# Kernel tuning notes

Measured on AMD Instinct MI355X. Metric: run time of the kernel, lower is better.

The kernel has to match this reference:

```python
import jax, jax.numpy as jnp
import numpy as np

N = 100000       # nodes
E = 1600000      # edges (before self-loops)
IN = 32          # input_dim
HID = 64         # hidden_dim
HEADS = 4
HO = HID // HEADS  # per-head out of gat1
OUT = 32         # output_dim
HID2 = HID // 2
BN_EPS = 1e-5
NEG_SLOPE = 0.2  # PyG GATConv default leaky relu slope


def setup_inputs() -> dict:
    key = jax.random.key(0)
    ks = jax.random.split(key, 28)
    f32 = jnp.float32
    rn = lambda k, s, sc=0.1: jax.random.normal(k, s, f32) * sc
    inp = {}
    inp["x"] = jax.random.normal(ks[0], (N, IN), f32)
    inp["edge_index"] = jax.random.randint(ks[1], (2, E), 0, N, jnp.int32)
    # GATConv 1: in=IN, heads=HEADS, out/head=HO, concat
    inp["W1"] = rn(ks[2], (IN, HEADS * HO))
    inp["att_src1"] = rn(ks[3], (HEADS, HO))
    inp["att_dst1"] = rn(ks[4], (HEADS, HO))
    inp["b1"] = rn(ks[5], (HEADS * HO,))
    # GATConv 2: in=HID, heads=1, out=OUT, no concat (mean)
    inp["W2"] = rn(ks[6], (HID, OUT))
    inp["att_src2"] = rn(ks[7], (1, OUT))
    inp["att_dst2"] = rn(ks[8], (1, OUT))
    inp["b2"] = rn(ks[9], (OUT,))
    # BatchNorms (inference mode: running stats)
    inp["bn1_g"] = jnp.ones((HID,), f32)
    inp["bn1_b"] = jnp.zeros((HID,), f32)
    inp["bn1_m"] = rn(ks[10], (HID,), 0.1)
    inp["bn1_v"] = jax.random.uniform(ks[11], (HID,), f32, 0.5, 1.5)
    inp["bn2_g"] = jnp.ones((OUT,), f32)
    inp["bn2_b"] = jnp.zeros((OUT,), f32)
    inp["bn2_m"] = rn(ks[12], (OUT,), 0.1)
    inp["bn2_v"] = jax.random.uniform(ks[13], (OUT,), f32, 0.5, 1.5)
    # classifier: OUT -> HID2 -> 3
    inp["cls_w1"] = rn(ks[14], (OUT, HID2))
    inp["cls_b1"] = rn(ks[15], (HID2,))
    inp["cls_w2"] = rn(ks[16], (HID2, 3))
    inp["cls_b2"] = rn(ks[17], (3,))
    inp["reg_w1"] = rn(ks[18], (OUT, HID2))
    inp["reg_b1"] = rn(ks[19], (HID2,))
    inp["reg_w2"] = rn(ks[20], (HID2, 1))
    inp["reg_b2"] = rn(ks[21], (1,))
    return inp


def _segment_softmax(e, seg, n):
    # e: [E, H]; softmax over edges sharing the same destination segment
    m = jax.ops.segment_max(e, seg, num_segments=n)
    ex = jnp.exp(e - m[seg])
    s = jax.ops.segment_sum(ex, seg, num_segments=n)
    return ex / (s[seg] + 1e-16)


def _gat(x, src, dst, W, a_src, a_dst, b, heads, ho, concat):
    n = x.shape[0]
    h = (x @ W).reshape(n, heads, ho)                    # [N,H,F]
    e = (h * a_src).sum(-1)[src] + (h * a_dst).sum(-1)[dst]  # [E,H]
    e = jax.nn.leaky_relu(e, NEG_SLOPE)
    alpha = _segment_softmax(e, dst, n)                  # [E,H]
    out = jax.ops.segment_sum(h[src] * alpha[:, :, None], dst, num_segments=n)
    out = out.reshape(n, heads * ho) if concat else out.mean(axis=1)
    return out + b


def _bn(x, g, b, m, v):
    return (x - m) * jax.lax.rsqrt(v + BN_EPS) * g + b


def reference(x, edge_index, W1, att_src1, att_dst1, b1, W2, att_src2, att_dst2, b2,
              bn1_g, bn1_b, bn1_m, bn1_v, bn2_g, bn2_b, bn2_m, bn2_v,
              cls_w1, cls_b1, cls_w2, cls_b2, reg_w1, reg_b1, reg_w2, reg_b2):
    n = x.shape[0]
    # PyG GATConv default add_self_loops=True
    loops = jnp.arange(n, dtype=edge_index.dtype)
    src = jnp.concatenate([edge_index[0], loops])
    dst = jnp.concatenate([edge_index[1], loops])

    h = _gat(x, src, dst, W1, att_src1, att_dst1, b1, HEADS, HO, True)   # [N, HID]
    h = jax.nn.relu(_bn(h, bn1_g, bn1_b, bn1_m, bn1_v))
    emb = _gat(h, src, dst, W2, att_src2, att_dst2, b2, 1, OUT, False)   # [N, OUT]
    emb = jax.nn.relu(_bn(emb, bn2_g, bn2_b, bn2_m, bn2_v))

    roles = jax.nn.relu(emb @ cls_w1 + cls_b1) @ cls_w2 + cls_b2          # [N, 3]
    energy = jax.nn.relu(emb @ reg_w1 + reg_b1) @ reg_w2 + reg_b2         # [N, 1]
    return emb, roles, energy
```

## Files before the change

kernel.cpp:

```cpp
#include <hip/hip_runtime.h>
#include <hip/hip_bf16.h>

#define NN 100000
#define EE 1600000
#define ETOT (EE + NN)
#define IND 32
#define HIDD 64
#define NHEADS 4
#define OUTD 32
#define HID2D 32
#define LOG2E 1.44269504f

#define BSH 8
#define NBUCK 391
#define CAP 5120
#define EPB 8192

typedef unsigned int uint;

__device__ __forceinline__ uint pack2(float a, float b) {
  uint lo = (uint)__bfloat16_as_ushort(__float2bfloat16(a));
  uint hi = (uint)__bfloat16_as_ushort(__float2bfloat16(b));
  return (hi << 16) | lo;
}
__device__ __forceinline__ float lo2f(uint w) { return __uint_as_float(w << 16); }
__device__ __forceinline__ float hi2r(uint w) { return __uint_as_float(w); }

__global__ __launch_bounds__(256) void k_lin1(
    const float* __restrict__ x, const float* __restrict__ W1,
    const float* __restrict__ atsrc, const float* __restrict__ atdst,
    uint* __restrict__ h1u, float* __restrict__ as1, float* __restrict__ ad1,
    int* __restrict__ bcur) {
  __shared__ float Ws[IND * HIDD];
  __shared__ float xs[8 * IND];
  __shared__ float atS[HIDD], atD[HIDD];
  int t = threadIdx.x;
  if (blockIdx.x == 0) { bcur[t] = 0; bcur[t + 256] = 0; }
  for (int i = t; i < IND * HIDD; i += 256) Ws[i] = W1[i];
  if (t < HIDD) { atS[t] = atsrc[t]; atD[t] = atdst[t]; }
  xs[t] = x[blockIdx.x * 256 + t];
  __syncthreads();
  int nl = t >> 5, tl = t & 31;
  int node = blockIdx.x * 8 + nl;
  int j0 = 2 * tl, j1 = j0 + 1;
  float a0 = 0.f, a1 = 0.f;
#pragma unroll
  for (int k = 0; k < IND; k++) {
    float xv = xs[nl * IND + k];
    a0 += xv * Ws[k * HIDD + j0];
    a1 += xv * Ws[k * HIDD + j1];
  }
  h1u[node * 32 + tl] = pack2(a0, a1);
  float ps = a0 * atS[j0] + a1 * atS[j1];
  float pd = a0 * atD[j0] + a1 * atD[j1];
#pragma unroll
  for (int off = 4; off >= 1; off >>= 1) {
    ps += __shfl_down(ps, off, 8);
    pd += __shfl_down(pd, off, 8);
  }
  if ((tl & 7) == 0) {
    as1[node * NHEADS + (tl >> 3)] = ps * LOG2E;
    ad1[node * NHEADS + (tl >> 3)] = pd * LOG2E;
  }
}

__global__ __launch_bounds__(256) void k_lin2(
    const float* __restrict__ hbn, const float* __restrict__ W2,
    const float* __restrict__ atsrc, const float* __restrict__ atdst,
    uint* __restrict__ h2u, float* __restrict__ as2, float* __restrict__ ad2) {
  __shared__ float Ws[HIDD * OUTD];
  __shared__ float xs[16 * HIDD];
  __shared__ float atS[OUTD], atD[OUTD];
  int t = threadIdx.x;
  for (int i = t; i < HIDD * OUTD; i += 256) Ws[i] = W2[i];
  if (t < OUTD) { atS[t] = atsrc[t]; atD[t] = atdst[t]; }
  for (int i = t; i < 16 * HIDD; i += 256) xs[i] = hbn[blockIdx.x * 16 * HIDD + i];
  __syncthreads();
  int nl = t >> 4, tl = t & 15;
  int node = blockIdx.x * 16 + nl;
  int j0 = 2 * tl, j1 = j0 + 1;
  float a0 = 0.f, a1 = 0.f;
#pragma unroll
  for (int k = 0; k < HIDD; k++) {
    float xv = xs[nl * HIDD + k];
    a0 += xv * Ws[k * OUTD + j0];
    a1 += xv * Ws[k * OUTD + j1];
  }
  h2u[node * 16 + tl] = pack2(a0, a1);
  float ps = a0 * atS[j0] + a1 * atS[j1];
  float pd = a0 * atD[j0] + a1 * atD[j1];
#pragma unroll
  for (int off = 8; off >= 1; off >>= 1) {
    ps += __shfl_down(ps, off, 16);
    pd += __shfl_down(pd, off, 16);
  }
  if (tl == 0) { as2[node] = ps * LOG2E; ad2[node] = pd * LOG2E; }
}

__global__ __launch_bounds__(256) void k_bin(const int* __restrict__ ei,
                                             int* __restrict__ bcur,
                                             int* __restrict__ bins) {
  __shared__ int cnt[NBUCK];
  int t = threadIdx.x;
  for (int i = t; i < NBUCK; i += 256) cnt[i] = 0;
  __syncthreads();
  int base = blockIdx.x * EPB;
  int lim = base + EPB; if (lim > ETOT) lim = ETOT;
  for (int i = base + t; i < lim; i += 256) {
    int d = (i < EE) ? ei[EE + i] : (i - EE);
    atomicAdd(&cnt[d >> BSH], 1);
  }
  __syncthreads();
  for (int i = t; i < NBUCK; i += 256) cnt[i] = atomicAdd(&bcur[i], cnt[i]);
  __syncthreads();
  for (int i = base + t; i < lim; i += 256) {
    int s, d;
    if (i < EE) { s = ei[i]; d = ei[EE + i]; } else { s = i - EE; d = s; }
    int bk = d >> BSH;
    int pos = atomicAdd(&cnt[bk], 1);
    bins[bk * CAP + pos] = (s << BSH) | (d & ((1 << BSH) - 1));
  }
}

__global__ __launch_bounds__(256) void k_csr(const int* __restrict__ bcur,
                                             const int* __restrict__ bins,
                                             int* __restrict__ rowp,
                                             int* __restrict__ srcs) {
  __shared__ int lrec[CAP];
  __shared__ int sA[512], sB[512];
  __shared__ int ldeg[256];
  int b = blockIdx.x, t = threadIdx.x;
  if (b == 0 && t == 0) rowp[NN] = ETOT;
  sA[t] = (t < NBUCK) ? bcur[t] : 0;
  sA[t + 256] = (t + 256 < NBUCK) ? bcur[t + 256] : 0;
  __syncthreads();
  int* in = sA; int* out = sB;
  for (int off = 1; off < 512; off <<= 1) {
    for (int i = t; i < 512; i += 256)
      out[i] = in[i] + ((i >= off) ? in[i - off] : 0);
    __syncthreads();
    int* tmp = in; in = out; out = tmp;
  }
  int gb = (b == 0) ? 0 : in[b - 1];
  __syncthreads();
  int count = bcur[b]; if (count > CAP) count = CAP;
  ldeg[t] = 0;
  __syncthreads();
  for (int i = t; i < count; i += 256) {
    int r = bins[b * CAP + i];
    lrec[i] = r;
    atomicAdd(&ldeg[r & 255], 1);
  }
  __syncthreads();
  int dv = ldeg[t];
  sA[t] = dv;
  __syncthreads();
  in = sA; out = sB;
  for (int off = 1; off < 256; off <<= 1) {
    out[t] = in[t] + ((t >= off) ? in[t - off] : 0);
    __syncthreads();
    int* tmp = in; in = out; out = tmp;
  }
  int nb = b << BSH;
  int ex = in[t] - dv;
  if (nb + t < NN) rowp[nb + t] = gb + ex;
  ldeg[t] = ex;
  __syncthreads();
  for (int i = t; i < count; i += 256) {
    int r = lrec[i];
    int pos = atomicAdd(&ldeg[r & 255], 1);
    srcs[gb + pos] = (r >> BSH) << 3;
  }
}

__global__ __launch_bounds__(256, 4) void k_agg1(
    const int* __restrict__ rowp, const int* __restrict__ srcs,
    const uint* __restrict__ h1u, const float* __restrict__ as1,
    const float* __restrict__ ad1, const float* __restrict__ b1,
    const float* __restrict__ g, const float* __restrict__ bb,
    const float* __restrict__ m, const float* __restrict__ v,
    float* __restrict__ hbn) {
  int t = threadIdx.x;
  int wid = t >> 6, lane = t & 63;
  int n0 = blockIdx.x * 16 + wid * 4;
  int slot = lane >> 3;
  int fl = lane & 7;
  int hd = fl >> 1;
  int rp[5];
#pragma unroll
  for (int k = 0; k < 5; k++) rp[k] = rowp[n0 + k];
  const uint4* h14 = (const uint4*)h1u;
  float acc[4][8], l[4], adv[4], as[4];
  int p[4], p1[4], lp[4], en[4], s1v[4];
  uint4 w[4];
#pragma unroll
  for (int k = 0; k < 4; k++) {
    adv[k] = ad1[(n0 + k) * NHEADS + hd];
    en[k] = rp[k + 1];
    lp[k] = en[k] - 1;
    p[k] = rp[k] + slot;
    int pc = p[k] < lp[k] ? p[k] : lp[k];
    int s0 = srcs[pc];
    w[k] = h14[s0 + fl];
    as[k] = as1[(s0 >> 1) + hd];
    p1[k] = p[k] + 8;
    int pc1 = p1[k] < lp[k] ? p1[k] : lp[k];
    s1v[k] = srcs[pc1];
    l[k] = 0.f;
#pragma unroll
    for (int i = 0; i < 8; i++) acc[k][i] = 0.f;
  }
  while (p[0] < en[0] || p[1] < en[1] || p[2] < en[2] || p[3] < en[3]) {
    uint4 wn[4]; float an[4]; int s2[4];
#pragma unroll
    for (int k = 0; k < 4; k++) {
      wn[k] = h14[s1v[k] + fl];
      an[k] = as1[(s1v[k] >> 1) + hd];
      int p2 = p1[k] + 8;
      int pc = p2 < lp[k] ? p2 : lp[k];
      s2[k] = srcs[pc];
    }
#pragma unroll
    for (int k = 0; k < 4; k++) {
      if (p[k] < en[k]) {
        float e = as[k] + adv[k];
        e = fmaxf(e, 0.2f * e);
        float ex = exp2f(e);
        l[k] += ex;
        acc[k][0] += ex * lo2f(w[k].x); acc[k][1] += ex * hi2r(w[k].x);
        acc[k][2] += ex * lo2f(w[k].y); acc[k][3] += ex * hi2r(w[k].y);
        acc[k][4] += ex * lo2f(w[k].z); acc[k][5] += ex * hi2r(w[k].z);
        acc[k][6] += ex * lo2f(w[k].w); acc[k][7] += ex * hi2r(w[k].w);
      }
      w[k] = wn[k]; as[k] = an[k]; s1v[k] = s2[k];
      p[k] = p1[k]; p1[k] += 8;
    }
  }
#pragma unroll
  for (int off = 8; off <= 32; off <<= 1) {
#pragma unroll
    for (int k = 0; k < 4; k++) {
#pragma unroll
      for (int i = 0; i < 8; i++) acc[k][i] += __shfl_xor(acc[k][i], off, 64);
      l[k] += __shfl_xor(l[k], off, 64);
    }
  }
  if (slot < 4) {
    float lsum = 0.f, av[8];
#pragma unroll
    for (int i = 0; i < 8; i++) av[i] = 0.f;
#pragma unroll
    for (int k = 0; k < 4; k++) {
      if (slot == k) {
        lsum = l[k];
#pragma unroll
        for (int i = 0; i < 8; i++) av[i] = acc[k][i];
      }
    }
    int node = n0 + slot;
    float li = 1.f / (lsum + 1e-16f);
    int fb = fl * 8;
    float o[8];
#pragma unroll
    for (int i = 0; i < 8; i++) {
      int j = fb + i;
      float ov = av[i] * li + b1[j];
      ov = (ov - m[j]) * rsqrtf(v[j] + 1e-5f) * g[j] + bb[j];
      o[i] = fmaxf(ov, 0.f);
    }
    float4* dst = (float4*)(hbn + node * HIDD + fb);
    dst[0] = make_float4(o[0], o[1], o[2], o[3]);
    dst[1] = make_float4(o[4], o[5], o[6], o[7]);
  }
}

__global__ __launch_bounds__(256, 4) void k_agg2(
    const int* __restrict__ rowp, const int* __restrict__ srcs,
    const uint* __restrict__ h2u, const float* __restrict__ as2,
    const float* __restrict__ ad2, const float* __restrict__ b2v,
    const float* __restrict__ g, const float* __restrict__ bb,
    const float* __restrict__ m, const float* __restrict__ v,
    float* __restrict__ out_emb) {
  int t = threadIdx.x;
  int wid = t >> 6, lane = t & 63;
  int n0 = blockIdx.x * 16 + wid * 4;
  int slot = lane >> 3;
  int fl = lane & 7;
  int rp[5];
#pragma unroll
  for (int k = 0; k < 5; k++) rp[k] = rowp[n0 + k];
  const uint2* h22 = (const uint2*)h2u;
  float acc[4][4], l[4], adv[4], as[4];
  int p[4], p1[4], lp[4], en[4], s1v[4];
  uint2 w[4];
#pragma unroll
  for (int k = 0; k < 4; k++) {
    adv[k] = ad2[n0 + k];
    en[k] = rp[k + 1];
    lp[k] = en[k] - 1;
    p[k] = rp[k] + slot;
    int pc = p[k] < lp[k] ? p[k] : lp[k];
    int s0 = srcs[pc];
    w[k] = h22[s0 + fl];
    as[k] = as2[s0 >> 3];
    p1[k] = p[k] + 8;
    int pc1 = p1[k] < lp[k] ? p1[k] : lp[k];
    s1v[k] = srcs[pc1];
    l[k] = 0.f;
#pragma unroll
    for (int i = 0; i < 4; i++) acc[k][i] = 0.f;
  }
  while (p[0] < en[0] || p[1] < en[1] || p[2] < en[2] || p[3] < en[3]) {
    uint2 wn[4]; float an[4]; int s2[4];
#pragma unroll
    for (int k = 0; k < 4; k++) {
      wn[k] = h22[s1v[k] + fl];
      an[k] = as2[s1v[k] >> 3];
      int p2 = p1[k] + 8;
      int pc = p2 < lp[k] ? p2 : lp[k];
      s2[k] = srcs[pc];
    }
#pragma unroll
    for (int k = 0; k < 4; k++) {
      if (p[k] < en[k]) {
        float e = as[k] + adv[k];
        e = fmaxf(e, 0.2f * e);
        float ex = exp2f(e);
        l[k] += ex;
        acc[k][0] += ex * lo2f(w[k].x); acc[k][1] += ex * hi2r(w[k].x);
        acc[k][2] += ex * lo2f(w[k].y); acc[k][3] += ex * hi2r(w[k].y);
      }
      w[k] = wn[k]; as[k] = an[k]; s1v[k] = s2[k];
      p[k] = p1[k]; p1[k] += 8;
    }
  }
#pragma unroll
  for (int off = 8; off <= 32; off <<= 1) {
#pragma unroll
    for (int k = 0; k < 4; k++) {
#pragma unroll
      for (int i = 0; i < 4; i++) acc[k][i] += __shfl_xor(acc[k][i], off, 64);
      l[k] += __shfl_xor(l[k], off, 64);
    }
  }
  if (slot < 4) {
    float lsum = 0.f, av[4];
#pragma unroll
    for (int i = 0; i < 4; i++) av[i] = 0.f;
#pragma unroll
    for (int k = 0; k < 4; k++) {
      if (slot == k) {
        lsum = l[k];
#pragma unroll
        for (int i = 0; i < 4; i++) av[i] = acc[k][i];
      }
    }
    int node = n0 + slot;
    float li = 1.f / (lsum + 1e-16f);
    int fb = fl * 4;
    float o[4];
#pragma unroll
    for (int i = 0; i < 4; i++) {
      int j = fb + i;
      float ov = av[i] * li + b2v[j];
      ov = (ov - m[j]) * rsqrtf(v[j] + 1e-5f) * g[j] + bb[j];
      o[i] = fmaxf(ov, 0.f);
    }
    *(float4*)(out_emb + node * OUTD + fb) = make_float4(o[0], o[1], o[2], o[3]);
  }
}

__global__ __launch_bounds__(256) void k_mlp(
    const float* __restrict__ embf,
    const float* __restrict__ cw1, const float* __restrict__ cb1,
    const float* __restrict__ cw2, const float* __restrict__ cb2,
    const float* __restrict__ rw1, const float* __restrict__ rb1,
    const float* __restrict__ rw2, const float* __restrict__ rb2,
    float* __restrict__ out_roles, float* __restrict__ out_energy) {
  __shared__ float C1[OUTD * HID2D], R1[OUTD * HID2D];
  __shared__ float C2[HID2D * 3], CB1[HID2D], RB1[HID2D], R2[HID2D];
  __shared__ float CB2v[3], RB2v;
  int t = threadIdx.x;
  for (int i = t; i < OUTD * HID2D; i += 256) { C1[i] = cw1[i]; R1[i] = rw1[i]; }
  if (t < HID2D) { CB1[t] = cb1[t]; RB1[t] = rb1[t]; R2[t] = rw2[t]; }
  if (t < HID2D * 3) C2[t] = cw2[t];
  if (t < 3) CB2v[t] = cb2[t];
  if (t == 0) RB2v = rb2[0];
  __syncthreads();
  int node = blockIdx.x * 256 + t;
  if (node >= NN) return;
  float e[OUTD];
#pragma unroll
  for (int k = 0; k < OUTD; k++) e[k] = embf[node * OUTD + k];
  float r0 = CB2v[0], r1 = CB2v[1], r2 = CB2v[2], en = RB2v;
  for (int j = 0; j < HID2D; j++) {
    float hc = CB1[j], hr = RB1[j];
#pragma unroll
    for (int k = 0; k < OUTD; k++) {
      hc += e[k] * C1[k * HID2D + j];
      hr += e[k] * R1[k * HID2D + j];
    }
    hc = fmaxf(hc, 0.f);
    hr = fmaxf(hr, 0.f);
    r0 += hc * C2[j * 3 + 0];
    r1 += hc * C2[j * 3 + 1];
    r2 += hc * C2[j * 3 + 2];
    en += hr * R2[j];
  }
  out_roles[node * 3 + 0] = r0;
  out_roles[node * 3 + 1] = r1;
  out_roles[node * 3 + 2] = r2;
  out_energy[node] = en;
}

extern "C" void kernel_launch(void* const* d_in, const int* in_sizes, int n_in,
                              void* d_out, int out_size, void* d_ws, size_t ws_size,
                              hipStream_t stream) {
  const float* x    = (const float*)d_in[0];
  const int*   ei   = (const int*)d_in[1];
  const float* W1   = (const float*)d_in[2];
  const float* as1w = (const float*)d_in[3];
  const float* ad1w = (const float*)d_in[4];
  const float* b1   = (const float*)d_in[5];
  const float* W2   = (const float*)d_in[6];
  const float* as2w = (const float*)d_in[7];
  const float* ad2w = (const float*)d_in[8];
  const float* b2v  = (const float*)d_in[9];
  const float* bn1g = (const float*)d_in[10];
  const float* bn1b = (const float*)d_in[11];
  const float* bn1m = (const float*)d_in[12];
  const float* bn1v = (const float*)d_in[13];
  const float* bn2g = (const float*)d_in[14];
  const float* bn2b = (const float*)d_in[15];
  const float* bn2m = (const float*)d_in[16];
  const float* bn2v = (const float*)d_in[17];
  const float* cw1  = (const float*)d_in[18];
  const float* cb1  = (const float*)d_in[19];
  const float* cw2  = (const float*)d_in[20];
  const float* cb2  = (const float*)d_in[21];
  const float* rw1  = (const float*)d_in[22];
  const float* rb1  = (const float*)d_in[23];
  const float* rw2  = (const float*)d_in[24];
  const float* rb2  = (const float*)d_in[25];

  uint*  h1u = (uint*)d_ws;
  float* hbn = (float*)(h1u + NN * 32);
  float* as1 = hbn + NN * HIDD;
  float* ad1 = as1 + NN * NHEADS;
  int* rowp  = (int*)(ad1 + NN * NHEADS);
  int* srcs  = rowp + NN + 1;
  int* bcur  = srcs + ETOT;
  int* bins  = bcur + 512;
  uint* h2u  = h1u;
  float* as2 = as1;
  float* ad2 = ad1;

  float* out        = (float*)d_out;
  float* out_emb    = out;
  float* out_roles  = out + NN * OUTD;
  float* out_energy = out + NN * (OUTD + 3);

  k_lin1<<<NN / 8, 256, 0, stream>>>(x, W1, as1w, ad1w, h1u, as1, ad1, bcur);
  k_bin<<<(ETOT + EPB - 1) / EPB, 256, 0, stream>>>(ei, bcur, bins);
  k_csr<<<NBUCK, 256, 0, stream>>>(bcur, bins, rowp, srcs);
  k_agg1<<<NN / 16, 256, 0, stream>>>(rowp, srcs, h1u, as1, ad1, b1, bn1g, bn1b, bn1m, bn1v, hbn);
  k_lin2<<<NN / 16, 256, 0, stream>>>(hbn, W2, as2w, ad2w, h2u, as2, ad2);
  k_agg2<<<NN / 16, 256, 0, stream>>>(rowp, srcs, h2u, as2, ad2, b2v, bn2g, bn2b, bn2m, bn2v, out_emb);
  k_mlp<<<(NN + 255) / 256, 256, 0, stream>>>(out_emb, cw1, cb1, cw2, cb2, rw1, rb1, rw2, rb2, out_roles, out_energy);
}
```

Baseline: 316.9 us.

## Build CSR with global degree atomics, two-pass scan, and atomic scatter

Result: slower. 475.9 us (+50.2%).

```diff
diff --git a/kernel.cpp b/kernel.cpp
--- a/kernel.cpp
+++ b/kernel.cpp
@@ -11,10 +11,9 @@
 #define HID2D 32
 #define LOG2E 1.44269504f
 
-#define BSH 8
-#define NBUCK 391
-#define CAP 5120
-#define EPB 8192
+#define NBK 391
+#define NNP (NBK * 256)
+#define EGRID ((ETOT + 1023) / 1024)
 
 typedef unsigned int uint;
 
@@ -30,12 +29,13 @@
     const float* __restrict__ x, const float* __restrict__ W1,
     const float* __restrict__ atsrc, const float* __restrict__ atdst,
     uint* __restrict__ h1u, float* __restrict__ as1, float* __restrict__ ad1,
-    int* __restrict__ bcur) {
+    int* __restrict__ deg) {
   __shared__ float Ws[IND * HIDD];
   __shared__ float xs[8 * IND];
   __shared__ float atS[HIDD], atD[HIDD];
   int t = threadIdx.x;
-  if (blockIdx.x == 0) { bcur[t] = 0; bcur[t + 256] = 0; }
+  if (t < 8) deg[(blockIdx.x << 3) + t] = 0;
+  if (blockIdx.x == 0 && t < (NNP - NN)) deg[NN + t] = 0;
   for (int i = t; i < IND * HIDD; i += 256) Ws[i] = W1[i];
   if (t < HIDD) { atS[t] = atsrc[t]; atD[t] = atdst[t]; }
   xs[t] = x[blockIdx.x * 256 + t];
@@ -97,42 +97,45 @@
   if (tl == 0) { as2[node] = ps * LOG2E; ad2[node] = pd * LOG2E; }
 }
 
-__global__ __launch_bounds__(256) void k_bin(const int* __restrict__ ei,
-                                             int* __restrict__ bcur,
-                                             int* __restrict__ bins) {
-  __shared__ int cnt[NBUCK];
-  int t = threadIdx.x;
-  for (int i = t; i < NBUCK; i += 256) cnt[i] = 0;
+__global__ __launch_bounds__(256) void k_deg(const int* __restrict__ ei,
+                                             int* __restrict__ deg) {
+  int i = blockIdx.x * 1024 + threadIdx.x;
+#pragma unroll
+  for (int u = 0; u < 4; u++, i += 256) {
+    if (i < ETOT) {
+      int d = (i < EE) ? ei[EE + i] : (i - EE);
+      atomicAdd(&deg[d], 1);
+    }
+  }
+}
+
+__global__ __launch_bounds__(256) void k_scan1(const int* __restrict__ deg,
+                                               int* __restrict__ lrow,
+                                               int* __restrict__ bsum) {
+  __shared__ int sA[256], sB[256];
+  int b = blockIdx.x, t = threadIdx.x;
+  int n = b * 256 + t;
+  int d = deg[n];
+  sA[t] = d;
   __syncthreads();
-  int base = blockIdx.x * EPB;
-  int lim = base + EPB; if (lim > ETOT) lim = ETOT;
-  for (int i = base + t; i < lim; i += 256) {
-    int d = (i < EE) ? ei[EE + i] : (i - EE);
-    atomicAdd(&cnt[d >> BSH], 1);
-  }
-  __syncthreads();
-  for (int i = t; i < NBUCK; i += 256) cnt[i] = atomicAdd(&bcur[i], cnt[i]);
-  __syncthreads();
-  for (int i = base + t; i < lim; i += 256) {
-    int s, d;
-    if (i < EE) { s = ei[i]; d = ei[EE + i]; } else { s = i - EE; d = s; }
-    int bk = d >> BSH;
-    int pos = atomicAdd(&cnt[bk], 1);
-    bins[bk * CAP + pos] = (s << BSH) | (d & ((1 << BSH) - 1));
-  }
-}
-
-__global__ __launch_bounds__(256) void k_csr(const int* __restrict__ bcur,
-                                             const int* __restrict__ bins,
-                                             int* __restrict__ rowp,
-                                             int* __restrict__ srcs) {
-  __shared__ int lrec[CAP];
+  int* in = sA; int* out = sB;
+  for (int off = 1; off < 256; off <<= 1) {
+    out[t] = in[t] + ((t >= off) ? in[t - off] : 0);
+    __syncthreads();
+    int* tmp = in; in = out; out = tmp;
+  }
+  lrow[n] = in[t] - d;
+  if (t == 255) bsum[b] = in[255];
+}
+
+__global__ __launch_bounds__(256) void k_scan2(const int* __restrict__ bsum,
+                                               const int* __restrict__ lrow,
+                                               int* __restrict__ rowp,
+                                               int* __restrict__ cur) {
   __shared__ int sA[512], sB[512];
-  __shared__ int ldeg[256];
   int b = blockIdx.x, t = threadIdx.x;
-  if (b == 0 && t == 0) rowp[NN] = ETOT;
-  sA[t] = (t < NBUCK) ? bcur[t] : 0;
-  sA[t + 256] = (t + 256 < NBUCK) ? bcur[t + 256] : 0;
+  sA[t] = (t < NBK) ? bsum[t] : 0;
+  sA[t + 256] = (t + 256 < NBK) ? bsum[t + 256] : 0;
   __syncthreads();
   int* in = sA; int* out = sB;
   for (int off = 1; off < 512; off <<= 1) {
@@ -142,34 +145,24 @@
     int* tmp = in; in = out; out = tmp;
   }
   int gb = (b == 0) ? 0 : in[b - 1];
-  __syncthreads();
-  int count = bcur[b]; if (count > CAP) count = CAP;
-  ldeg[t] = 0;
-  __syncthreads();
-  for (int i = t; i < count; i += 256) {
-    int r = bins[b * CAP + i];
-    lrec[i] = r;
-    atomicAdd(&ldeg[r & 255], 1);
-  }
-  __syncthreads();
-  int dv = ldeg[t];
-  sA[t] = dv;
-  __syncthreads();
-  in = sA; out = sB;
-  for (int off = 1; off < 256; off <<= 1) {
-    out[t] = in[t] + ((t >= off) ? in[t - off] : 0);
-    __syncthreads();
-    int* tmp = in; in = out; out = tmp;
-  }
-  int nb = b << BSH;
-  int ex = in[t] - dv;
-  if (nb + t < NN) rowp[nb + t] = gb + ex;
-  ldeg[t] = ex;
-  __syncthreads();
-  for (int i = t; i < count; i += 256) {
-    int r = lrec[i];
-    int pos = atomicAdd(&ldeg[r & 255], 1);
-    srcs[gb + pos] = (r >> BSH) << 3;
+  int n = b * 256 + t;
+  int v = gb + lrow[n];
+  if (n < NN) { rowp[n] = v; cur[n] = v; }
+  else if (n == NN) rowp[NN] = ETOT;
+}
+
+__global__ __launch_bounds__(256) void k_scat(const int* __restrict__ ei,
+                                              int* __restrict__ cur,
+                                              int* __restrict__ srcs) {
+  int i = blockIdx.x * 1024 + threadIdx.x;
+#pragma unroll
+  for (int u = 0; u < 4; u++, i += 256) {
+    if (i < ETOT) {
+      int s, d;
+      if (i < EE) { s = ei[i]; d = ei[EE + i]; } else { s = d = i - EE; }
+      int pos = atomicAdd(&cur[d], 1);
+      srcs[pos] = s << 3;
+    }
   }
 }
 
@@ -449,8 +442,10 @@
   float* ad1 = as1 + NN * NHEADS;
   int* rowp  = (int*)(ad1 + NN * NHEADS);
   int* srcs  = rowp + NN + 1;
-  int* bcur  = srcs + ETOT;
-  int* bins  = bcur + 512;
+  int* deg   = srcs + ETOT;
+  int* lrow  = deg + NNP;
+  int* cur   = lrow + NNP;
+  int* bsum  = cur + NNP;
   uint* h2u  = h1u;
   float* as2 = as1;
   float* ad2 = ad1;
@@ -460,9 +455,11 @@
   float* out_roles  = out + NN * OUTD;
   float* out_energy = out + NN * (OUTD + 3);
 
-  k_lin1<<<NN / 8, 256, 0, stream>>>(x, W1, as1w, ad1w, h1u, as1, ad1, bcur);
-  k_bin<<<(ETOT + EPB - 1) / EPB, 256, 0, stream>>>(ei, bcur, bins);
-  k_csr<<<NBUCK, 256, 0, stream>>>(bcur, bins, rowp, srcs);
+  k_lin1<<<NN / 8, 256, 0, stream>>>(x, W1, as1w, ad1w, h1u, as1, ad1, deg);
+  k_deg<<<EGRID, 256, 0, stream>>>(ei, deg);
+  k_scan1<<<NBK, 256, 0, stream>>>(deg, lrow, bsum);
+  k_scan2<<<NBK, 256, 0, stream>>>(bsum, lrow, rowp, cur);
+  k_scat<<<EGRID, 256, 0, stream>>>(ei, cur, srcs);
   k_agg1<<<NN / 16, 256, 0, stream>>>(rowp, srcs, h1u, as1, ad1, b1, bn1g, bn1b, bn1m, bn1v, hbn);
   k_lin2<<<NN / 16, 256, 0, stream>>>(hbn, W2, as2w, ad2w, h2u, as2, ad2);
   k_agg2<<<NN / 16, 256, 0, stream>>>(rowp, srcs, h2u, as2, ad2, b2v, bn2g, bn2b, bn2m, bn2v, out_emb);
```

## Fuse layer-2 linear projection into first aggregation epilogue

Applied to the files above, without the earlier changes.

After: 324.1 us. +2.3%, slower.

```diff
diff --git a/kernel.cpp b/kernel.cpp
--- a/kernel.cpp
+++ b/kernel.cpp
@@ -64,39 +64,6 @@
   }
 }
 
-__global__ __launch_bounds__(256) void k_lin2(
-    const float* __restrict__ hbn, const float* __restrict__ W2,
-    const float* __restrict__ atsrc, const float* __restrict__ atdst,
-    uint* __restrict__ h2u, float* __restrict__ as2, float* __restrict__ ad2) {
-  __shared__ float Ws[HIDD * OUTD];
-  __shared__ float xs[16 * HIDD];
-  __shared__ float atS[OUTD], atD[OUTD];
-  int t = threadIdx.x;
-  for (int i = t; i < HIDD * OUTD; i += 256) Ws[i] = W2[i];
-  if (t < OUTD) { atS[t] = atsrc[t]; atD[t] = atdst[t]; }
-  for (int i = t; i < 16 * HIDD; i += 256) xs[i] = hbn[blockIdx.x * 16 * HIDD + i];
-  __syncthreads();
-  int nl = t >> 4, tl = t & 15;
-  int node = blockIdx.x * 16 + nl;
-  int j0 = 2 * tl, j1 = j0 + 1;
-  float a0 = 0.f, a1 = 0.f;
-#pragma unroll
-  for (int k = 0; k < HIDD; k++) {
-    float xv = xs[nl * HIDD + k];
-    a0 += xv * Ws[k * OUTD + j0];
-    a1 += xv * Ws[k * OUTD + j1];
-  }
-  h2u[node * 16 + tl] = pack2(a0, a1);
-  float ps = a0 * atS[j0] + a1 * atS[j1];
-  float pd = a0 * atD[j0] + a1 * atD[j1];
-#pragma unroll
-  for (int off = 8; off >= 1; off >>= 1) {
-    ps += __shfl_down(ps, off, 16);
-    pd += __shfl_down(pd, off, 16);
-  }
-  if (tl == 0) { as2[node] = ps * LOG2E; ad2[node] = pd * LOG2E; }
-}
-
 __global__ __launch_bounds__(256) void k_bin(const int* __restrict__ ei,
                                              int* __restrict__ bcur,
                                              int* __restrict__ bins) {
@@ -179,8 +146,18 @@
     const float* __restrict__ ad1, const float* __restrict__ b1,
     const float* __restrict__ g, const float* __restrict__ bb,
     const float* __restrict__ m, const float* __restrict__ v,
-    float* __restrict__ hbn) {
+    const float* __restrict__ W2, const float* __restrict__ atsrc2,
+    const float* __restrict__ atdst2,
+    uint* __restrict__ h2u, float* __restrict__ as2, float* __restrict__ ad2) {
+  __shared__ float W2t[OUTD * HIDD];
+  __shared__ float atS2[OUTD], atD2[OUTD];
   int t = threadIdx.x;
+  for (int i = t; i < OUTD * HIDD; i += 256) {
+    int j = i >> 6, k = i & 63;
+    W2t[i] = W2[k * OUTD + j];
+  }
+  if (t < OUTD) { atS2[t] = atsrc2[t]; atD2[t] = atdst2[t]; }
+  __syncthreads();
   int wid = t >> 6, lane = t & 63;
   int n0 = blockIdx.x * 16 + wid * 4;
   int slot = lane >> 3;
@@ -245,32 +222,63 @@
       l[k] += __shfl_xor(l[k], off, 64);
     }
   }
-  if (slot < 4) {
-    float lsum = 0.f, av[8];
-#pragma unroll
-    for (int i = 0; i < 8; i++) av[i] = 0.f;
-#pragma unroll
-    for (int k = 0; k < 4; k++) {
-      if (slot == k) {
-        lsum = l[k];
-#pragma unroll
-        for (int i = 0; i < 8; i++) av[i] = acc[k][i];
-      }
-    }
-    int node = n0 + slot;
-    float li = 1.f / (lsum + 1e-16f);
-    int fb = fl * 8;
-    float o[8];
+  int s = slot & 3, half = slot >> 2;
+  int node = n0 + s;
+  float lsum = 0.f, av[8];
+#pragma unroll
+  for (int i = 0; i < 8; i++) av[i] = 0.f;
+#pragma unroll
+  for (int k = 0; k < 4; k++) {
+    if (s == k) {
+      lsum = l[k];
+#pragma unroll
+      for (int i = 0; i < 8; i++) av[i] = acc[k][i];
+    }
+  }
+  float li = 1.f / (lsum + 1e-16f);
+  int fb = fl * 8;
+  float o[8];
+#pragma unroll
+  for (int i = 0; i < 8; i++) {
+    int j = fb + i;
+    float ov = av[i] * li + b1[j];
+    ov = (ov - m[j]) * rsqrtf(v[j] + 1e-5f) * g[j] + bb[j];
+    o[i] = fmaxf(ov, 0.f);
+  }
+  float psel0 = 0.f, psel1 = 0.f, ps = 0.f, pd = 0.f;
+#pragma unroll
+  for (int r = 0; r < 8; r++) {
+    int jp = (half << 3) | r;
+    int j0 = jp * 2;
+    float a0 = 0.f, a1 = 0.f;
 #pragma unroll
     for (int i = 0; i < 8; i++) {
-      int j = fb + i;
-      float ov = av[i] * li + b1[j];
-      ov = (ov - m[j]) * rsqrtf(v[j] + 1e-5f) * g[j] + bb[j];
-      o[i] = fmaxf(ov, 0.f);
-    }
-    float4* dst = (float4*)(hbn + node * HIDD + fb);
-    dst[0] = make_float4(o[0], o[1], o[2], o[3]);
-    dst[1] = make_float4(o[4], o[5], o[6], o[7]);
+      a0 += o[i] * W2t[j0 * HIDD + fb + i];
+      a1 += o[i] * W2t[(j0 + 1) * HIDD + fb + i];
+    }
+#pragma unroll
+    for (int off = 1; off <= 4; off <<= 1) {
+      a0 += __shfl_xor(a0, off, 64);
+      a1 += __shfl_xor(a1, off, 64);
+    }
+    if (fl == r) {
+      psel0 = a0; psel1 = a1;
+      ps = a0 * atS2[j0] + a1 * atS2[j0 + 1];
+      pd = a0 * atD2[j0] + a1 * atD2[j0 + 1];
+    }
+  }
+  int jp = (half << 3) | fl;
+  h2u[node * 16 + jp] = pack2(psel0, psel1);
+#pragma unroll
+  for (int off = 1; off <= 4; off <<= 1) {
+    ps += __shfl_xor(ps, off, 64);
+    pd += __shfl_xor(pd, off, 64);
+  }
+  ps += __shfl_xor(ps, 32, 64);
+  pd += __shfl_xor(pd, 32, 64);
+  if (fl == 0 && half == 0) {
+    as2[node] = ps * LOG2E;
+    ad2[node] = pd * LOG2E;
   }
 }
 
@@ -444,16 +452,15 @@
   const float* rb2  = (const float*)d_in[25];
 
   uint*  h1u = (uint*)d_ws;
-  float* hbn = (float*)(h1u + NN * 32);
-  float* as1 = hbn + NN * HIDD;
+  uint*  h2u = h1u + NN * 32;
+  float* as1 = (float*)(h2u + NN * 16);
   float* ad1 = as1 + NN * NHEADS;
-  int* rowp  = (int*)(ad1 + NN * NHEADS);
+  float* as2 = ad1 + NN * NHEADS;
+  float* ad2 = as2 + NN;
+  int* rowp  = (int*)(ad2 + NN);
   int* srcs  = rowp + NN + 1;
   int* bcur  = srcs + ETOT;
   int* bins  = bcur + 512;
-  uint* h2u  = h1u;
-  float* as2 = as1;
-  float* ad2 = ad1;
 
   float* out        = (float*)d_out;
   float* out_emb    = out;
@@ -463,8 +470,8 @@
   k_lin1<<<NN / 8, 256, 0, stream>>>(x, W1, as1w, ad1w, h1u, as1, ad1, bcur);
   k_bin<<<(ETOT + EPB - 1) / EPB, 256, 0, stream>>>(ei, bcur, bins);
   k_csr<<<NBUCK, 256, 0, stream>>>(bcur, bins, rowp, srcs);
-  k_agg1<<<NN / 16, 256, 0, stream>>>(rowp, srcs, h1u, as1, ad1, b1, bn1g, bn1b, bn1m, bn1v, hbn);
-  k_lin2<<<NN / 16, 256, 0, stream>>>(hbn, W2, as2w, ad2w, h2u, as2, ad2);
+  k_agg1<<<NN / 16, 256, 0, stream>>>(rowp, srcs, h1u, as1, ad1, b1, bn1g, bn1b, bn1m, bn1v,
+                                      W2, as2w, ad2w, h2u, as2, ad2);
   k_agg2<<<NN / 16, 256, 0, stream>>>(rowp, srcs, h2u, as2, ad2, b2v, bn2g, bn2b, bn2m, bn2v, out_emb);
   k_mlp<<<(NN + 255) / 256, 256, 0, stream>>>(out_emb, cw1, cb1, cw2, cb2, rw1, rb1, rw2, rb2, out_roles, out_energy);
 }
```

## Register-tile the second GAT linear layer with a transposed, swizzled shared-memory input tile

Applied to the files above, without the earlier changes.

New measurement: 383.2 us. 1.21x slower.

```diff
diff --git a/kernel.cpp b/kernel.cpp
--- a/kernel.cpp
+++ b/kernel.cpp
@@ -15,6 +15,7 @@
 #define NBUCK 391
 #define CAP 5120
 #define EPB 8192
+#define L2NB 128
 
 typedef unsigned int uint;
 
@@ -62,39 +63,6 @@
     as1[node * NHEADS + (tl >> 3)] = ps * LOG2E;
     ad1[node * NHEADS + (tl >> 3)] = pd * LOG2E;
   }
-}
-
-__global__ __launch_bounds__(256) void k_lin2(
-    const float* __restrict__ hbn, const float* __restrict__ W2,
-    const float* __restrict__ atsrc, const float* __restrict__ atdst,
-    uint* __restrict__ h2u, float* __restrict__ as2, float* __restrict__ ad2) {
-  __shared__ float Ws[HIDD * OUTD];
-  __shared__ float xs[16 * HIDD];
-  __shared__ float atS[OUTD], atD[OUTD];
-  int t = threadIdx.x;
-  for (int i = t; i < HIDD * OUTD; i += 256) Ws[i] = W2[i];
-  if (t < OUTD) { atS[t] = atsrc[t]; atD[t] = atdst[t]; }
-  for (int i = t; i < 16 * HIDD; i += 256) xs[i] = hbn[blockIdx.x * 16 * HIDD + i];
-  __syncthreads();
-  int nl = t >> 4, tl = t & 15;
-  int node = blockIdx.x * 16 + nl;
-  int j0 = 2 * tl, j1 = j0 + 1;
-  float a0 = 0.f, a1 = 0.f;
-#pragma unroll
-  for (int k = 0; k < HIDD; k++) {
-    float xv = xs[nl * HIDD + k];
-    a0 += xv * Ws[k * OUTD + j0];
-    a1 += xv * Ws[k * OUTD + j1];
-  }
-  h2u[node * 16 + tl] = pack2(a0, a1);
-  float ps = a0 * atS[j0] + a1 * atS[j1];
-  float pd = a0 * atD[j0] + a1 * atD[j1];
-#pragma unroll
-  for (int off = 8; off >= 1; off >>= 1) {
-    ps += __shfl_down(ps, off, 16);
-    pd += __shfl_down(pd, off, 16);
-  }
-  if (tl == 0) { as2[node] = ps * LOG2E; ad2[node] = pd * LOG2E; }
 }
 
 __global__ __launch_bounds__(256) void k_bin(const int* __restrict__ ei,
@@ -271,6 +239,76 @@
     float4* dst = (float4*)(hbn + node * HIDD + fb);
     dst[0] = make_float4(o[0], o[1], o[2], o[3]);
     dst[1] = make_float4(o[4], o[5], o[6], o[7]);
+  }
+}
+
+__global__ __launch_bounds__(256) void k_lin2(
+    const float* __restrict__ hbn, const float* __restrict__ W2,
+    const float* __restrict__ atsrc, const float* __restrict__ atdst,
+    uint* __restrict__ h2u, float* __restrict__ as2, float* __restrict__ ad2) {
+  __shared__ float xsT[HIDD][L2NB];
+  __shared__ float Wp[HIDD * OUTD];
+  __shared__ float atS[OUTD], atD[OUTD];
+  int t = threadIdx.x;
+  int nb = blockIdx.x * L2NB;
+  for (int i = t; i < HIDD * OUTD; i += 256) Wp[i] = W2[i];
+  if (t < OUTD) { atS[t] = atsrc[t]; atD[t] = atdst[t]; }
+#pragma unroll
+  for (int i = 0; i < 8; i++) {
+    int idx = t + i * 256;
+    int node = idx >> 4, c = idx & 15;
+    int gnode = nb + node;
+    float4 vv = make_float4(0.f, 0.f, 0.f, 0.f);
+    if (gnode < NN) vv = ((const float4*)hbn)[gnode * 16 + c];
+    int ns = node ^ ((c & 7) << 2);
+    xsT[4 * c + 0][ns] = vv.x;
+    xsT[4 * c + 1][ns] = vv.y;
+    xsT[4 * c + 2][ns] = vv.z;
+    xsT[4 * c + 3][ns] = vv.w;
+  }
+  __syncthreads();
+  int w = t >> 6, lane = t & 63;
+  int gq = lane >> 3, tl = lane & 7;
+  int base = w * 32 + gq * 4;
+  int j0 = tl * 4;
+  float acc[4][4];
+#pragma unroll
+  for (int e = 0; e < 4; e++)
+#pragma unroll
+    for (int d = 0; d < 4; d++) acc[e][d] = 0.f;
+#pragma unroll
+  for (int k = 0; k < HIDD; k++) {
+    float4 wv = *(const float4*)&Wp[k * OUTD + j0];
+    int swz = ((k >> 2) & 7) << 2;
+    float4 xv = *(const float4*)&xsT[k][base ^ swz];
+    acc[0][0] += xv.x * wv.x; acc[0][1] += xv.x * wv.y;
+    acc[0][2] += xv.x * wv.z; acc[0][3] += xv.x * wv.w;
+    acc[1][0] += xv.y * wv.x; acc[1][1] += xv.y * wv.y;
+    acc[1][2] += xv.y * wv.z; acc[1][3] += xv.y * wv.w;
+    acc[2][0] += xv.z * wv.x; acc[2][1] += xv.z * wv.y;
+    acc[2][2] += xv.z * wv.z; acc[2][3] += xv.z * wv.w;
+    acc[3][0] += xv.w * wv.x; acc[3][1] += xv.w * wv.y;
+    acc[3][2] += xv.w * wv.z; acc[3][3] += xv.w * wv.w;
+  }
+#pragma unroll
+  for (int e = 0; e < 4; e++) {
+    int node = nb + base + e;
+    float ps = acc[e][0] * atS[j0] + acc[e][1] * atS[j0 + 1] +
+               acc[e][2] * atS[j0 + 2] + acc[e][3] * atS[j0 + 3];
+    float pd = acc[e][0] * atD[j0] + acc[e][1] * atD[j0 + 1] +
+               acc[e][2] * atD[j0 + 2] + acc[e][3] * atD[j0 + 3];
+#pragma unroll
+    for (int off = 1; off <= 4; off <<= 1) {
+      ps += __shfl_xor(ps, off, 64);
+      pd += __shfl_xor(pd, off, 64);
+    }
+    if (node < NN) {
+      uint2 pk;
+      pk.x = pack2(acc[e][0], acc[e][1]);
+      pk.y = pack2(acc[e][2], acc[e][3]);
+      ((uint2*)h2u)[node * 8 + tl] = pk;
+      if (tl == 0) { as2[node] = ps * LOG2E; ad2[node] = pd * LOG2E; }
+    }
   }
 }
 
@@ -464,7 +502,7 @@
   k_bin<<<(ETOT + EPB - 1) / EPB, 256, 0, stream>>>(ei, bcur, bins);
   k_csr<<<NBUCK, 256, 0, stream>>>(bcur, bins, rowp, srcs);
   k_agg1<<<NN / 16, 256, 0, stream>>>(rowp, srcs, h1u, as1, ad1, b1, bn1g, bn1b, bn1m, bn1v, hbn);
-  k_lin2<<<NN / 16, 256, 0, stream>>>(hbn, W2, as2w, ad2w, h2u, as2, ad2);
+  k_lin2<<<(NN + L2NB - 1) / L2NB, 256, 0, stream>>>(hbn, W2, as2w, ad2w, h2u, as2, ad2);
   k_agg2<<<NN / 16, 256, 0, stream>>>(rowp, srcs, h2u, as2, ad2, b2v, bn2g, bn2b, bn2m, bn2v, out_emb);
   k_mlp<<<(NN + 255) / 256, 256, 0, stream>>>(out_emb, cw1, cb1, cw2, cb2, rw1, rb1, rw2, rb2, out_roles, out_energy);
 }
```
